# Kernel optimization log

Measured on AMD Instinct MI355X. Metric: run time of the kernel, lower is better.

Reference implementation:

```python
import jax, jax.numpy as jnp
import numpy as np

COMMITMENT_COST = 0.25


def l2norm(x, eps=1e-12):
    # F.normalize along last dim
    n = jnp.linalg.norm(x, axis=-1, keepdims=True)
    return x / jnp.maximum(n, eps)


def vector_quantize(x, codebook, commitment_cost):
    """Euclidean VQ: cdist + argmin, straight-through, VQ loss + perplexity.
    x: (B, N, D), codebook: (K, D)."""
    B, N, D = x.shape
    K = codebook.shape[0]
    flat = x.reshape(-1, D)  # (BN, D)
    # squared euclidean distances via expansion (no (BN,K,D) intermediate)
    d = (jnp.sum(flat * flat, axis=-1, keepdims=True)
         - 2.0 * flat @ codebook.T
         + jnp.sum(codebook * codebook, axis=-1))  # (BN, K)
    idx = jnp.argmin(d, axis=-1)  # (BN,)
    q = codebook[idx]  # (BN, D)
    # VQ losses
    e_latent = jnp.mean((jax.lax.stop_gradient(q) - flat) ** 2)
    q_latent = jnp.mean((q - jax.lax.stop_gradient(flat)) ** 2)
    loss = q_latent + commitment_cost * e_latent
    # perplexity over codebook usage (bincount, not dense one-hot)
    counts = jnp.zeros((K,), flat.dtype).at[idx].add(1.0)
    probs = counts / idx.shape[0]
    perplexity = jnp.exp(-jnp.sum(probs * jnp.log(probs + 1e-10)))
    return idx.reshape(B, N), perplexity, loss


def transform_mfcc(X):
    # wave_embedding.transform_freq: normalize frames, then rfft -> real -> bins 2:40
    Xn = l2norm(X)
    spec = jnp.fft.rfft(Xn, axis=-1).real[..., 2:40]  # (B, N, 38)
    return l2norm(spec)  # mfcc_embedding.norm_fn


def setup_inputs() -> dict:
    key = jax.random.key(0)
    k1, k2, k3 = jax.random.split(key, 3)
    X = jax.random.normal(k1, (16, 4096, 80), dtype=jnp.float32)
    wave_codebook = jax.random.normal(k2, (1024, 80), dtype=jnp.float32)
    mfcc_codebook = jax.random.normal(k3, (256, 38), dtype=jnp.float32)
    return {"X": X, "wave_codebook": wave_codebook, "mfcc_codebook": mfcc_codebook}


def reference(X, wave_codebook, mfcc_codebook):
    K_wave = wave_codebook.shape[0]
    wave_idx, wave_ppl, wave_loss = vector_quantize(X, wave_codebook, COMMITMENT_COST)
    X_mfcc = transform_mfcc(X)
    mfcc_idx, mfcc_ppl, mfcc_loss = vector_quantize(X_mfcc, mfcc_codebook, COMMITMENT_COST)
    mfcc_idx = mfcc_idx + K_wave
    # rearrange stack([wave, mfcc], dim=1): 'b c n -> b (n c)' -> interleave per frame
    B, N = wave_idx.shape
    encodings = jnp.stack([wave_idx, mfcc_idx], axis=-1).reshape(B, 2 * N)
    return encodings, wave_ppl, wave_loss, mfcc_ppl, mfcc_loss
```

## Files before the change

kernel.cpp:

```cpp
#include <hip/hip_runtime.h>
#include <hip/hip_bf16.h>
#include <math.h>


#define NROWS 65536
#define DW    80
#define KW    1024
#define DM    38
#define KM    256

typedef __attribute__((ext_vector_type(8))) short bf16x8;
typedef __attribute__((ext_vector_type(4))) float f32x4;

__device__ __forceinline__ void bf16split(float v, short& h, short& l) {
    __hip_bfloat16 hb = __float2bfloat16(v);
    float hf = __bfloat162float(hb);
    __hip_bfloat16 lb = __float2bfloat16(v - hf);
    h = *(short*)&hb;
    l = *(short*)&lb;
}

__device__ __forceinline__ void bf16split3(float v, short& a, short& b, short& c) {
    __hip_bfloat16 h = __float2bfloat16(v);
    float hf = __bfloat162float(h);
    float r = v - hf;
    __hip_bfloat16 m = __float2bfloat16(r);
    float mf = __bfloat162float(m);
    __hip_bfloat16 lo = __float2bfloat16(r - mf);
    a = *(short*)&h; b = *(short*)&m; c = *(short*)&lo;
}

__device__ __forceinline__ bf16x8 bf8zero() {
    bf16x8 z;
    #pragma unroll
    for (int j = 0; j < 8; ++j) z[j] = 0;
    return z;
}

__device__ __forceinline__ void wvq_tile(
    const bf16x8 (&Ah)[4][3], const bf16x8 (&Al)[4][3],
    const bf16x8 (&bh)[3], const bf16x8 (&bl)[3],
    float cnv, int idx0, float (&bd)[4][4], int (&bi)[4][4])
{
    f32x4 aL[4], aH[4];
    #pragma unroll
    for (int rt = 0; rt < 4; ++rt) {
        aL[rt] = (f32x4){0.f, 0.f, 0.f, 0.f};
        aH[rt] = (f32x4){0.f, 0.f, 0.f, 0.f};
    }
    #pragma unroll
    for (int s = 0; s < 3; ++s) {
        #pragma unroll
        for (int rt = 0; rt < 4; ++rt)
            aL[rt] = __builtin_amdgcn_mfma_f32_16x16x32_bf16(Al[rt][s], bl[s], aL[rt], 0, 0, 0);
        #pragma unroll
        for (int rt = 0; rt < 4; ++rt)
            aL[rt] = __builtin_amdgcn_mfma_f32_16x16x32_bf16(Ah[rt][s], bl[s], aL[rt], 0, 0, 0);
        #pragma unroll
        for (int rt = 0; rt < 4; ++rt)
            aH[rt] = __builtin_amdgcn_mfma_f32_16x16x32_bf16(Al[rt][s], bh[s], aH[rt], 0, 0, 0);
        #pragma unroll
        for (int rt = 0; rt < 4; ++rt)
            aH[rt] = __builtin_amdgcn_mfma_f32_16x16x32_bf16(Ah[rt][s], bh[s], aH[rt], 0, 0, 0);
    }
    #pragma unroll
    for (int rt = 0; rt < 4; ++rt)
        #pragma unroll
        for (int i = 0; i < 4; ++i) {
            float d = fmaf(-2.f, aL[rt][i] + aH[rt][i], cnv);
            if (d < bd[rt][i]) { bd[rt][i] = d; bi[rt][i] = idx0; }
        }
}

#define WS_SUMS   0
#define WS_HIST   256
#define WS_CNW    5376
#define WS_CNM    9472
#define WS_CTF    10496
#define WS_CBF    33536
#define WS_CWH    107264
#define WS_CWL    303872

__global__ __launch_bounds__(256) void prep_kernel(
    const float* __restrict__ cbw, const float* __restrict__ cbm,
    float* __restrict__ sums, int* __restrict__ hist,
    float* __restrict__ cn_w, float* __restrict__ cn_m,
    short* __restrict__ ctf, short* __restrict__ cbf,
    short* __restrict__ cwh, short* __restrict__ cwl)
{
    int idx = blockIdx.x * 256 + threadIdx.x;
    if (idx < 12288) {
        const int f = idx;
        const int ct = f / 192, rem = f % 192, s = rem >> 6, l = rem & 63;
        const int code = ct * 16 + (l & 15);
        const int k0 = 32 * s + 8 * (l >> 4);
        bf16x8 h, lo;
        if (k0 < DW) {
            const float4* p = (const float4*)(cbw + (size_t)code * DW + k0);
            float4 u = p[0], v = p[1];
            float fv[8] = {u.x, u.y, u.z, u.w, v.x, v.y, v.z, v.w};
            #pragma unroll
            for (int j = 0; j < 8; ++j) {
                short hh, ll;
                bf16split(fv[j], hh, ll);
                h[j] = hh; lo[j] = ll;
            }
        } else { h = bf8zero(); lo = bf8zero(); }
        *(bf16x8*)&cwh[(size_t)f * 8] = h;
        *(bf16x8*)&cwl[(size_t)f * 8] = lo;
    } else if (idx < 16128) {
        int t = idx - 12288;
        int col, k;
        if (t < 3072) {
            int j = t & 7, l = (t >> 3) & 63, tt = t >> 9;
            col = (tt >> 1) * 16 + (l & 15);
            k = 32 * (tt & 1) + 8 * (l >> 4) + j;
        } else {
            int i2 = t - 3072;
            int j = i2 & 7, l = (i2 >> 3) & 31, ct = i2 >> 8;
            col = ct * 16 + (l & 15);
            k = 64 + 8 * (l >> 4) + j;
        }
        float v = (col < DM)
            ? (float)cos(2.0 * 3.14159265358979323846 * (double)((col + 2) * k) / 80.0)
            : 0.f;
        short a, b, c; bf16split3(v, a, b, c);
        ctf[t] = a; ctf[3840 + t] = b; ctf[7680 + t] = c;
    } else if (idx < 28416) {
        int i3 = idx - 16128;
        int code, k;
        if (i3 < 8192) {
            int j = i3 & 7, l = (i3 >> 3) & 63, ct = i3 >> 9;
            code = ct * 16 + (l & 15);
            k = 8 * (l >> 4) + j;
        } else {
            int i4 = i3 - 8192;
            int j = i4 & 7, l = (i4 >> 3) & 31, ct = i4 >> 8;
            code = ct * 16 + (l & 15);
            k = 32 + 8 * (l >> 4) + j;
        }
        float v = (k < DM) ? cbm[(size_t)code * DM + k] : 0.f;
        short a, b, c; bf16split3(v, a, b, c);
        cbf[i3] = a; cbf[12288 + i3] = b; cbf[24576 + i3] = c;
    } else if (idx < 29440) {
        int i = idx - 28416;
        const float* p = cbw + (size_t)i * DW;
        float s = 0.f;
        for (int k = 0; k < DW; ++k) s = fmaf(p[k], p[k], s);
        cn_w[i] = s;
    } else if (idx < 29696) {
        int i = idx - 29440;
        const float* p = cbm + (size_t)i * DM;
        float s = 0.f;
        for (int j = 0; j < DM; ++j) s = fmaf(p[j], p[j], s);
        cn_m[i] = s;
    } else if (idx < 30976) {
        hist[idx - 29696] = 0;
    } else if (idx == 30976) sums[0] = 0.f;
    else if (idx == 30977)   sums[1] = 0.f;
}

__global__ __launch_bounds__(256, 2) void wave_vq_mfma(
    const float* __restrict__ X, const short* __restrict__ cwh,
    const short* __restrict__ cwl, const float* __restrict__ cn,
    float* __restrict__ out, float* __restrict__ sums)
{
    __shared__ float sd[2][64][16];
    __shared__ int   si[2][64][16];
    __shared__ float redw[2];

    const int tid  = threadIdx.x;
    const int l    = tid & 63;
    const int qu   = tid >> 6;
    const int grp  = qu >> 1;
    const int half = qu & 1;
    const int c16  = l & 15;
    const int g    = l >> 4;
    const size_t rowbase = (size_t)blockIdx.x * 128 + (size_t)grp * 64;

    bf16x8 Ah[4][3], Al[4][3];
    float xs2[4] = {0.f, 0.f, 0.f, 0.f};
    #pragma unroll
    for (int rt = 0; rt < 4; ++rt) {
        #pragma unroll
        for (int s = 0; s < 3; ++s) {
            const int k0 = 32 * s + 8 * g;
            bf16x8 ah, al;
            if (k0 < DW) {
                const float4* ap =
                    (const float4*)(X + (rowbase + rt * 16 + c16) * DW + k0);
                float4 u = ap[0], w = ap[1];
                float f[8] = {u.x, u.y, u.z, u.w, w.x, w.y, w.z, w.w};
                #pragma unroll
                for (int j = 0; j < 8; ++j) {
                    short hh, ll;
                    bf16split(f[j], hh, ll);
                    ah[j] = hh; al[j] = ll;
                    xs2[rt] = fmaf(f[j], f[j], xs2[rt]);
                }
            } else {
                ah = bf8zero(); al = bf8zero();
            }
            Ah[rt][s] = ah; Al[rt][s] = al;
        }
    }
    #pragma unroll
    for (int rt = 0; rt < 4; ++rt) {
        xs2[rt] += __shfl_xor(xs2[rt], 16, 64);
        xs2[rt] += __shfl_xor(xs2[rt], 32, 64);
    }

    float bd[4][4];
    int   bi[4][4];
    #pragma unroll
    for (int rt = 0; rt < 4; ++rt)
        #pragma unroll
        for (int i = 0; i < 4; ++i) { bd[rt][i] = 3.4e38f; bi[rt][i] = 0; }

    const bf16x8* Hp = (const bf16x8*)cwh + l;
    const bf16x8* Lp = (const bf16x8*)cwl + l;
    const int ct0 = half * 32;

    bf16x8 b0h[3], b0l[3], b1h[3], b1l[3];
    float cn0, cn1;
    #pragma unroll
    for (int s = 0; s < 3; ++s) {
        b0h[s] = Hp[(ct0 * 3 + s) * 64];
        b0l[s] = Lp[(ct0 * 3 + s) * 64];
    }
    cn0 = cn[ct0 * 16 + c16];

    #pragma unroll 1
    for (int ctl = 0; ctl < 32; ctl += 2) {
        const int ct = ct0 + ctl;
        #pragma unroll
        for (int s = 0; s < 3; ++s) {
            b1h[s] = Hp[((ct + 1) * 3 + s) * 64];
            b1l[s] = Lp[((ct + 1) * 3 + s) * 64];
        }
        cn1 = cn[(ct + 1) * 16 + c16];
        wvq_tile(Ah, Al, b0h, b0l, cn0, ct * 16 + c16, bd, bi);
        if (ctl + 2 < 32) {
            #pragma unroll
            for (int s = 0; s < 3; ++s) {
                b0h[s] = Hp[((ct + 2) * 3 + s) * 64];
                b0l[s] = Lp[((ct + 2) * 3 + s) * 64];
            }
            cn0 = cn[(ct + 2) * 16 + c16];
        }
        wvq_tile(Ah, Al, b1h, b1l, cn1, (ct + 1) * 16 + c16, bd, bi);
    }

    if (half == 1) {
        #pragma unroll
        for (int rt = 0; rt < 4; ++rt)
            #pragma unroll
            for (int i = 0; i < 4; ++i) {
                sd[grp][l][rt * 4 + i] = bd[rt][i];
                si[grp][l][rt * 4 + i] = bi[rt][i];
            }
    }
    __syncthreads();
    if (half == 0) {
        float lw = 0.f;
        #pragma unroll
        for (int rt = 0; rt < 4; ++rt) {
            #pragma unroll
            for (int i = 0; i < 4; ++i) {
                float d = bd[rt][i]; int ix = bi[rt][i];
                float dp = sd[grp][l][rt * 4 + i];
                int   ip = si[grp][l][rt * 4 + i];
                if (dp < d || (dp == d && ip < ix)) { d = dp; ix = ip; }
                #pragma unroll
                for (int m = 1; m < 16; m <<= 1) {
                    float d2 = __shfl_xor(d, m, 64);
                    int   i2 = __shfl_xor(ix, m, 64);
                    if (d2 < d || (d2 == d && i2 < ix)) { d = d2; ix = i2; }
                }
                float xn = __shfl(xs2[rt], (l & 48) + 4 * (l >> 4) + i, 64);
                if (c16 == 0) {
                    size_t row = rowbase + rt * 16 + 4 * g + i;
                    out[2 * row] = (float)ix;
                    lw += d + xn;
                }
            }
        }
        #pragma unroll
        for (int m = 1; m < 64; m <<= 1) lw += __shfl_xor(lw, m, 64);
        if (l == 0) redw[grp] = lw;
    }
    __syncthreads();
    if (tid == 0) atomicAdd(&sums[0], redw[0] + redw[1]);
}

__global__ __launch_bounds__(256, 2) void mfcc_mfma(
    const float* __restrict__ X, const float* __restrict__ cn_m,
    const short* __restrict__ ctf, const short* __restrict__ cbf,
    float* __restrict__ out, float* __restrict__ sums)
{
    __shared__ float XF[2][64 * 49];
    __shared__ float sd[2][64][16];
    __shared__ int   si[2][64][16];
    __shared__ float CN[KM];
    __shared__ float red2[2];

    const int tid  = threadIdx.x;
    const int l    = tid & 63;
    const int qu   = tid >> 6;
    const int grp  = qu >> 1;
    const int half = qu & 1;
    const int c16  = l & 15;
    const int g    = l >> 4;
    const size_t rowbase = (size_t)blockIdx.x * 128 + (size_t)grp * 64;

    CN[tid] = cn_m[tid];

    float* xfl = &XF[grp][0];

    #pragma unroll 1
    for (int rt2 = 0; rt2 < 2; ++rt2) {
        const int rt = half * 2 + rt2;
        bf16x8 A0[3], A1[3], A2[3];
        #pragma unroll
        for (int s = 0; s < 3; ++s) {
            const int k0 = 32 * s + 8 * g;
            if (k0 < DW) {
                const float4* ap =
                    (const float4*)(X + (rowbase + rt * 16 + c16) * DW + k0);
                float4 u = ap[0], v = ap[1];
                float f[8] = {u.x, u.y, u.z, u.w, v.x, v.y, v.z, v.w};
                bf16x8 a0, a1, a2;
                #pragma unroll
                for (int j = 0; j < 8; ++j) {
                    short aa, bb, cc;
                    bf16split3(f[j], aa, bb, cc);
                    a0[j] = aa; a1[j] = bb; a2[j] = cc;
                }
                A0[s] = a0; A1[s] = a1; A2[s] = a2;
            } else {
                A0[s] = bf8zero(); A1[s] = bf8zero(); A2[s] = bf8zero();
            }
        }

        f32x4 accA[3], accB[3];
        #pragma unroll
        for (int ct = 0; ct < 3; ++ct) {
            accA[ct] = (f32x4){0.f, 0.f, 0.f, 0.f};
            accB[ct] = (f32x4){0.f, 0.f, 0.f, 0.f};
        }

        #pragma unroll
        for (int s = 0; s < 3; ++s) {
            #pragma unroll
            for (int ct = 0; ct < 3; ++ct) {
                bf16x8 b0, b1, b2;
                if (s < 2) {
                    const int off = ((ct * 2 + s) * 64 + l) * 8;
                    b0 = *(const bf16x8*)&ctf[off];
                    b1 = *(const bf16x8*)&ctf[3840 + off];
                    b2 = *(const bf16x8*)&ctf[7680 + off];
                } else if (l < 32) {
                    const int off = 3072 + (ct * 32 + l) * 8;
                    b0 = *(const bf16x8*)&ctf[off];
                    b1 = *(const bf16x8*)&ctf[3840 + off];
                    b2 = *(const bf16x8*)&ctf[7680 + off];
                } else {
                    b0 = bf8zero(); b1 = bf8zero(); b2 = bf8zero();
                }
                accA[ct] = __builtin_amdgcn_mfma_f32_16x16x32_bf16(A2[s], b0, accA[ct], 0, 0, 0);
                accA[ct] = __builtin_amdgcn_mfma_f32_16x16x32_bf16(A1[s], b1, accA[ct], 0, 0, 0);
                accA[ct] = __builtin_amdgcn_mfma_f32_16x16x32_bf16(A0[s], b2, accA[ct], 0, 0, 0);
                accB[ct] = __builtin_amdgcn_mfma_f32_16x16x32_bf16(A1[s], b0, accB[ct], 0, 0, 0);
                accB[ct] = __builtin_amdgcn_mfma_f32_16x16x32_bf16(A0[s], b1, accB[ct], 0, 0, 0);
                accB[ct] = __builtin_amdgcn_mfma_f32_16x16x32_bf16(A0[s], b0, accB[ct], 0, 0, 0);
            }
        }

        f32x4 acc[3];
        #pragma unroll
        for (int ct = 0; ct < 3; ++ct) acc[ct] = accA[ct] + accB[ct];

        #pragma unroll
        for (int i = 0; i < 4; ++i) {
            float n2 = acc[0][i] * acc[0][i];
            n2 = fmaf(acc[1][i], acc[1][i], n2);
            n2 = fmaf(acc[2][i], acc[2][i], n2);
            #pragma unroll
            for (int m = 1; m < 16; m <<= 1) n2 += __shfl_xor(n2, m, 64);
            float inv = 1.0f / fmaxf(sqrtf(n2), 1e-12f);
            const int row_l = rt * 16 + 4 * g + i;
            #pragma unroll
            for (int ct = 0; ct < 3; ++ct)
                xfl[row_l * 49 + ct * 16 + c16] = acc[ct][i] * inv;
        }
    }
    __syncthreads();

    bf16x8 X0[4][3], X1[4][3];
    #pragma unroll
    for (int rt = 0; rt < 4; ++rt) {
        const int r0 = rt * 16 + c16;
        {
            const float* p = &xfl[r0 * 49 + 8 * g];
            bf16x8 q0, q1, q2;
            #pragma unroll
            for (int j = 0; j < 8; ++j) {
                short aa, bb, cc;
                bf16split3(p[j], aa, bb, cc);
                q0[j] = aa; q1[j] = bb; q2[j] = cc;
            }
            X0[rt][0] = q0; X0[rt][1] = q1; X0[rt][2] = q2;
        }
        if (g < 2) {
            const float* p = &xfl[r0 * 49 + 32 + 8 * g];
            bf16x8 q0, q1, q2;
            #pragma unroll
            for (int j = 0; j < 8; ++j) {
                short aa, bb, cc;
                bf16split3(p[j], aa, bb, cc);
                q0[j] = aa; q1[j] = bb; q2[j] = cc;
            }
            X1[rt][0] = q0; X1[rt][1] = q1; X1[rt][2] = q2;
        } else {
            X1[rt][0] = bf8zero(); X1[rt][1] = bf8zero(); X1[rt][2] = bf8zero();
        }
    }

    float bd[4][4];
    int   bi[4][4];
    #pragma unroll
    for (int rt = 0; rt < 4; ++rt)
        #pragma unroll
        for (int i = 0; i < 4; ++i) { bd[rt][i] = 3.4e38f; bi[rt][i] = 0; }

    #pragma unroll 1
    for (int ctl = 0; ctl < 8; ++ctl) {
        const int ct = half * 8 + ctl;
        bf16x8 B0[3], B1[3];
        const int off0 = (ct * 64 + l) * 8;
        B0[0] = *(const bf16x8*)&cbf[off0];
        B0[1] = *(const bf16x8*)&cbf[12288 + off0];
        B0[2] = *(const bf16x8*)&cbf[24576 + off0];
        if (l < 32) {
            const int off1 = 8192 + (ct * 32 + l) * 8;
            B1[0] = *(const bf16x8*)&cbf[off1];
            B1[1] = *(const bf16x8*)&cbf[12288 + off1];
            B1[2] = *(const bf16x8*)&cbf[24576 + off1];
        } else {
            B1[0] = bf8zero(); B1[1] = bf8zero(); B1[2] = bf8zero();
        }
        const float cnv = CN[ct * 16 + c16];
        const int idxbase = ct * 16 + c16;
        #pragma unroll
        for (int rt = 0; rt < 4; ++rt) {
            f32x4 p0 = (f32x4){0.f, 0.f, 0.f, 0.f};
            f32x4 q0 = (f32x4){0.f, 0.f, 0.f, 0.f};
            f32x4 p1 = (f32x4){0.f, 0.f, 0.f, 0.f};
            f32x4 q1 = (f32x4){0.f, 0.f, 0.f, 0.f};
            p0 = __builtin_amdgcn_mfma_f32_16x16x32_bf16(X0[rt][2], B0[0], p0, 0, 0, 0);
            p0 = __builtin_amdgcn_mfma_f32_16x16x32_bf16(X0[rt][1], B0[1], p0, 0, 0, 0);
            p0 = __builtin_amdgcn_mfma_f32_16x16x32_bf16(X0[rt][0], B0[2], p0, 0, 0, 0);
            q0 = __builtin_amdgcn_mfma_f32_16x16x32_bf16(X0[rt][1], B0[0], q0, 0, 0, 0);
            q0 = __builtin_amdgcn_mfma_f32_16x16x32_bf16(X0[rt][0], B0[1], q0, 0, 0, 0);
            q0 = __builtin_amdgcn_mfma_f32_16x16x32_bf16(X0[rt][0], B0[0], q0, 0, 0, 0);
            p1 = __builtin_amdgcn_mfma_f32_16x16x32_bf16(X1[rt][2], B1[0], p1, 0, 0, 0);
            p1 = __builtin_amdgcn_mfma_f32_16x16x32_bf16(X1[rt][1], B1[1], p1, 0, 0, 0);
            p1 = __builtin_amdgcn_mfma_f32_16x16x32_bf16(X1[rt][0], B1[2], p1, 0, 0, 0);
            q1 = __builtin_amdgcn_mfma_f32_16x16x32_bf16(X1[rt][1], B1[0], q1, 0, 0, 0);
            q1 = __builtin_amdgcn_mfma_f32_16x16x32_bf16(X1[rt][0], B1[1], q1, 0, 0, 0);
            q1 = __builtin_amdgcn_mfma_f32_16x16x32_bf16(X1[rt][0], B1[0], q1, 0, 0, 0);
            #pragma unroll
            for (int i = 0; i < 4; ++i) {
                float d = fmaf(-2.f, (p0[i] + q0[i]) + (p1[i] + q1[i]), cnv);
                if (d < bd[rt][i]) { bd[rt][i] = d; bi[rt][i] = idxbase; }
            }
        }
    }

    if (half == 1) {
        #pragma unroll
        for (int rt = 0; rt < 4; ++rt)
            #pragma unroll
            for (int i = 0; i < 4; ++i) {
                sd[grp][l][rt * 4 + i] = bd[rt][i];
                si[grp][l][rt * 4 + i] = bi[rt][i];
            }
    }
    __syncthreads();
    if (half == 0) {
        float lm = 0.f;
        #pragma unroll
        for (int rt = 0; rt < 4; ++rt) {
            #pragma unroll
            for (int i = 0; i < 4; ++i) {
                float d = bd[rt][i]; int ix = bi[rt][i];
                float dp = sd[grp][l][rt * 4 + i];
                int   ip = si[grp][l][rt * 4 + i];
                if (dp < d || (dp == d && ip < ix)) { d = dp; ix = ip; }
                #pragma unroll
                for (int m = 1; m < 16; m <<= 1) {
                    float d2 = __shfl_xor(d, m, 64);
                    int   i2 = __shfl_xor(ix, m, 64);
                    if (d2 < d || (d2 == d && i2 < ix)) { d = d2; ix = i2; }
                }
                if (c16 == 0) {
                    size_t row = rowbase + rt * 16 + 4 * g + i;
                    out[2 * row + 1] = (float)(ix + KW);
                    lm += d + 1.0f;
                }
            }
        }
        #pragma unroll
        for (int m = 1; m < 64; m <<= 1) lm += __shfl_xor(lm, m, 64);
        if (l == 0) red2[grp] = lm;
    }
    __syncthreads();
    if (tid == 0) atomicAdd(&sums[1], red2[0] + red2[1]);
}

__global__ __launch_bounds__(256) void hist_kernel(
    const float* __restrict__ out, int* __restrict__ hist)
{
    __shared__ int h[1280];
    const int tid = threadIdx.x;
    for (int i = tid; i < 1280; i += 256) h[i] = 0;
    __syncthreads();
    const int r = blockIdx.x * 256 + tid;
    float2 e = *(const float2*)&out[2 * r];
    atomicAdd(&h[(int)e.x], 1);
    atomicAdd(&h[1024 + ((int)e.y - KW)], 1);
    __syncthreads();
    for (int i = tid; i < 1280; i += 256)
        if (h[i]) atomicAdd(&hist[i], h[i]);
}

__global__ __launch_bounds__(256) void finalize_kernel(
    const int* __restrict__ hist, const float* __restrict__ sums,
    float* __restrict__ out)
{
    __shared__ float red[4];
    const int tid = threadIdx.x;
    const bool wv = (blockIdx.x == 0);
    const int K = wv ? KW : KM;
    const int base = wv ? 0 : 1024;
    float s = 0.f;
    for (int i = tid; i < K; i += 256) {
        float p = (float)hist[base + i] * (1.0f / 65536.0f);
        s += p * logf(p + 1e-10f);
    }
    #pragma unroll
    for (int off = 32; off >= 1; off >>= 1) s += __shfl_xor(s, off, 64);
    if ((tid & 63) == 0) red[tid >> 6] = s;
    __syncthreads();
    if (tid == 0) {
        float t = red[0] + red[1] + red[2] + red[3];
        float ppl = expf(-t);
        float denom = wv ? (float)(NROWS * DW) : (float)(NROWS * DM);
        int obase = 2 * NROWS + (wv ? 0 : 2);
        out[obase]     = ppl;
        out[obase + 1] = 1.25f * sums[wv ? 0 : 1] / denom;
    }
}

extern "C" void kernel_launch(void* const* d_in, const int* in_sizes, int n_in,
                              void* d_out, int out_size, void* d_ws, size_t ws_size,
                              hipStream_t stream) {
    const float* X   = (const float*)d_in[0];
    const float* cbw = (const float*)d_in[1];
    const float* cbm = (const float*)d_in[2];
    float* out = (float*)d_out;

    char* ws = (char*)d_ws;
    float* sums = (float*)(ws + WS_SUMS);
    int*   hist = (int*)(ws + WS_HIST);
    float* cn_w = (float*)(ws + WS_CNW);
    float* cn_m = (float*)(ws + WS_CNM);
    short* ctf  = (short*)(ws + WS_CTF);
    short* cbf  = (short*)(ws + WS_CBF);
    short* cwh  = (short*)(ws + WS_CWH);
    short* cwl  = (short*)(ws + WS_CWL);

    prep_kernel<<<122, 256, 0, stream>>>(cbw, cbm, sums, hist, cn_w, cn_m,
                                         ctf, cbf, cwh, cwl);
    wave_vq_mfma<<<NROWS / 128, 256, 0, stream>>>(X, cwh, cwl, cn_w, out, sums);
    mfcc_mfma<<<NROWS / 128, 256, 0, stream>>>(X, cn_m, ctf, cbf, out, sums);
    hist_kernel<<<NROWS / 256, 256, 0, stream>>>(out, hist);
    finalize_kernel<<<2, 256, 0, stream>>>(hist, sums, out);
}
```

Measured before the change: 95.28 us.

## Stage wave codebook tiles in LDS and split rows across all four waves

The wave VQ kernel no longer splits the codebook between two half-waves per 64-row group. Each of the four waves now owns 32 rows and scans the full codebook. Codebook hi/lo tiles are loaded cooperatively into shared memory in chunks of four column tiles, with register prefetch of the next chunk. This removes redundant per-wave global codebook loads and the cross-half LDS argmin merge. In exchange it adds per-chunk block barriers and halves the rows per wave, which lowers MFMA reuse of each loaded B fragment.

```diff
diff --git a/kernel.cpp b/kernel.cpp
--- a/kernel.cpp
+++ b/kernel.cpp
@@ -37,34 +37,34 @@
     return z;
 }
 
-__device__ __forceinline__ void wvq_tile(
-    const bf16x8 (&Ah)[4][3], const bf16x8 (&Al)[4][3],
+__device__ __forceinline__ void wvq_tile2(
+    const bf16x8 (&Ah)[2][3], const bf16x8 (&Al)[2][3],
     const bf16x8 (&bh)[3], const bf16x8 (&bl)[3],
-    float cnv, int idx0, float (&bd)[4][4], int (&bi)[4][4])
+    float cnv, int idx0, float (&bd)[2][4], int (&bi)[2][4])
 {
-    f32x4 aL[4], aH[4];
-    #pragma unroll
-    for (int rt = 0; rt < 4; ++rt) {
+    f32x4 aL[2], aH[2];
+    #pragma unroll
+    for (int rt = 0; rt < 2; ++rt) {
         aL[rt] = (f32x4){0.f, 0.f, 0.f, 0.f};
         aH[rt] = (f32x4){0.f, 0.f, 0.f, 0.f};
     }
     #pragma unroll
     for (int s = 0; s < 3; ++s) {
         #pragma unroll
-        for (int rt = 0; rt < 4; ++rt)
+        for (int rt = 0; rt < 2; ++rt)
             aL[rt] = __builtin_amdgcn_mfma_f32_16x16x32_bf16(Al[rt][s], bl[s], aL[rt], 0, 0, 0);
         #pragma unroll
-        for (int rt = 0; rt < 4; ++rt)
+        for (int rt = 0; rt < 2; ++rt)
             aL[rt] = __builtin_amdgcn_mfma_f32_16x16x32_bf16(Ah[rt][s], bl[s], aL[rt], 0, 0, 0);
         #pragma unroll
-        for (int rt = 0; rt < 4; ++rt)
+        for (int rt = 0; rt < 2; ++rt)
             aH[rt] = __builtin_amdgcn_mfma_f32_16x16x32_bf16(Al[rt][s], bh[s], aH[rt], 0, 0, 0);
         #pragma unroll
-        for (int rt = 0; rt < 4; ++rt)
+        for (int rt = 0; rt < 2; ++rt)
             aH[rt] = __builtin_amdgcn_mfma_f32_16x16x32_bf16(Ah[rt][s], bh[s], aH[rt], 0, 0, 0);
     }
     #pragma unroll
-    for (int rt = 0; rt < 4; ++rt)
+    for (int rt = 0; rt < 2; ++rt)
         #pragma unroll
         for (int i = 0; i < 4; ++i) {
             float d = fmaf(-2.f, aL[rt][i] + aH[rt][i], cnv);
@@ -165,23 +165,21 @@
     const short* __restrict__ cwl, const float* __restrict__ cn,
     float* __restrict__ out, float* __restrict__ sums)
 {
-    __shared__ float sd[2][64][16];
-    __shared__ int   si[2][64][16];
-    __shared__ float redw[2];
-
-    const int tid  = threadIdx.x;
-    const int l    = tid & 63;
-    const int qu   = tid >> 6;
-    const int grp  = qu >> 1;
-    const int half = qu & 1;
-    const int c16  = l & 15;
-    const int g    = l >> 4;
-    const size_t rowbase = (size_t)blockIdx.x * 128 + (size_t)grp * 64;
-
-    bf16x8 Ah[4][3], Al[4][3];
-    float xs2[4] = {0.f, 0.f, 0.f, 0.f};
-    #pragma unroll
-    for (int rt = 0; rt < 4; ++rt) {
+    __shared__ int4 LH4[768];
+    __shared__ int4 LL4[768];
+    __shared__ float redw[4];
+
+    const int tid = threadIdx.x;
+    const int l   = tid & 63;
+    const int qu  = tid >> 6;
+    const int c16 = l & 15;
+    const int g   = l >> 4;
+    const size_t rowbase = (size_t)blockIdx.x * 128 + (size_t)qu * 32;
+
+    bf16x8 Ah[2][3], Al[2][3];
+    float xs2[2] = {0.f, 0.f};
+    #pragma unroll
+    for (int rt = 0; rt < 2; ++rt) {
         #pragma unroll
         for (int s = 0; s < 3; ++s) {
             const int k0 = 32 * s + 8 * g;
@@ -205,92 +203,92 @@
         }
     }
     #pragma unroll
-    for (int rt = 0; rt < 4; ++rt) {
+    for (int rt = 0; rt < 2; ++rt) {
         xs2[rt] += __shfl_xor(xs2[rt], 16, 64);
         xs2[rt] += __shfl_xor(xs2[rt], 32, 64);
     }
 
-    float bd[4][4];
-    int   bi[4][4];
-    #pragma unroll
-    for (int rt = 0; rt < 4; ++rt)
+    float bd[2][4];
+    int   bi[2][4];
+    #pragma unroll
+    for (int rt = 0; rt < 2; ++rt)
         #pragma unroll
         for (int i = 0; i < 4; ++i) { bd[rt][i] = 3.4e38f; bi[rt][i] = 0; }
 
-    const bf16x8* Hp = (const bf16x8*)cwh + l;
-    const bf16x8* Lp = (const bf16x8*)cwl + l;
-    const int ct0 = half * 32;
-
-    bf16x8 b0h[3], b0l[3], b1h[3], b1l[3];
-    float cn0, cn1;
-    #pragma unroll
-    for (int s = 0; s < 3; ++s) {
-        b0h[s] = Hp[(ct0 * 3 + s) * 64];
-        b0l[s] = Lp[(ct0 * 3 + s) * 64];
-    }
-    cn0 = cn[ct0 * 16 + c16];
+    const int4* Hg = (const int4*)cwh;
+    const int4* Lg = (const int4*)cwl;
+
+    int4 rh[3], rl[3];
+    #pragma unroll
+    for (int i = 0; i < 3; ++i) {
+        rh[i] = Hg[i * 256 + tid];
+        rl[i] = Lg[i * 256 + tid];
+    }
+    #pragma unroll
+    for (int i = 0; i < 3; ++i) {
+        LH4[i * 256 + tid] = rh[i];
+        LL4[i * 256 + tid] = rl[i];
+    }
+    __syncthreads();
 
     #pragma unroll 1
-    for (int ctl = 0; ctl < 32; ctl += 2) {
-        const int ct = ct0 + ctl;
-        #pragma unroll
-        for (int s = 0; s < 3; ++s) {
-            b1h[s] = Hp[((ct + 1) * 3 + s) * 64];
-            b1l[s] = Lp[((ct + 1) * 3 + s) * 64];
-        }
-        cn1 = cn[(ct + 1) * 16 + c16];
-        wvq_tile(Ah, Al, b0h, b0l, cn0, ct * 16 + c16, bd, bi);
-        if (ctl + 2 < 32) {
+    for (int c = 0; c < 16; ++c) {
+        if (c + 1 < 16) {
+            #pragma unroll
+            for (int i = 0; i < 3; ++i) {
+                rh[i] = Hg[(c + 1) * 768 + i * 256 + tid];
+                rl[i] = Lg[(c + 1) * 768 + i * 256 + tid];
+            }
+        }
+        #pragma unroll
+        for (int t = 0; t < 4; ++t) {
+            const int ct = c * 4 + t;
+            bf16x8 bh[3], bl[3];
             #pragma unroll
             for (int s = 0; s < 3; ++s) {
-                b0h[s] = Hp[((ct + 2) * 3 + s) * 64];
-                b0l[s] = Lp[((ct + 2) * 3 + s) * 64];
-            }
-            cn0 = cn[(ct + 2) * 16 + c16];
-        }
-        wvq_tile(Ah, Al, b1h, b1l, cn1, (ct + 1) * 16 + c16, bd, bi);
-    }
-
-    if (half == 1) {
-        #pragma unroll
-        for (int rt = 0; rt < 4; ++rt)
-            #pragma unroll
-            for (int i = 0; i < 4; ++i) {
-                sd[grp][l][rt * 4 + i] = bd[rt][i];
-                si[grp][l][rt * 4 + i] = bi[rt][i];
-            }
-    }
-    __syncthreads();
-    if (half == 0) {
-        float lw = 0.f;
-        #pragma unroll
-        for (int rt = 0; rt < 4; ++rt) {
-            #pragma unroll
-            for (int i = 0; i < 4; ++i) {
-                float d = bd[rt][i]; int ix = bi[rt][i];
-                float dp = sd[grp][l][rt * 4 + i];
-                int   ip = si[grp][l][rt * 4 + i];
-                if (dp < d || (dp == d && ip < ix)) { d = dp; ix = ip; }
-                #pragma unroll
-                for (int m = 1; m < 16; m <<= 1) {
-                    float d2 = __shfl_xor(d, m, 64);
-                    int   i2 = __shfl_xor(ix, m, 64);
-                    if (d2 < d || (d2 == d && i2 < ix)) { d = d2; ix = i2; }
-                }
-                float xn = __shfl(xs2[rt], (l & 48) + 4 * (l >> 4) + i, 64);
-                if (c16 == 0) {
-                    size_t row = rowbase + rt * 16 + 4 * g + i;
-                    out[2 * row] = (float)ix;
-                    lw += d + xn;
-                }
-            }
-        }
-        #pragma unroll
-        for (int m = 1; m < 64; m <<= 1) lw += __shfl_xor(lw, m, 64);
-        if (l == 0) redw[grp] = lw;
-    }
-    __syncthreads();
-    if (tid == 0) atomicAdd(&sums[0], redw[0] + redw[1]);
+                bh[s] = *(const bf16x8*)&LH4[(t * 3 + s) * 64 + l];
+                bl[s] = *(const bf16x8*)&LL4[(t * 3 + s) * 64 + l];
+            }
+            const float cnv = cn[ct * 16 + c16];
+            wvq_tile2(Ah, Al, bh, bl, cnv, ct * 16 + c16, bd, bi);
+        }
+        __syncthreads();
+        if (c + 1 < 16) {
+            #pragma unroll
+            for (int i = 0; i < 3; ++i) {
+                LH4[i * 256 + tid] = rh[i];
+                LL4[i * 256 + tid] = rl[i];
+            }
+            __syncthreads();
+        }
+    }
+
+    float lw = 0.f;
+    #pragma unroll
+    for (int rt = 0; rt < 2; ++rt) {
+        #pragma unroll
+        for (int i = 0; i < 4; ++i) {
+            float d = bd[rt][i]; int ix = bi[rt][i];
+            #pragma unroll
+            for (int m = 1; m < 16; m <<= 1) {
+                float d2 = __shfl_xor(d, m, 64);
+                int   i2 = __shfl_xor(ix, m, 64);
+                if (d2 < d || (d2 == d && i2 < ix)) { d = d2; ix = i2; }
+            }
+            float xn = __shfl(xs2[rt], (l & 48) + 4 * g + i, 64);
+            if (c16 == 0) {
+                size_t row = rowbase + rt * 16 + 4 * g + i;
+                out[2 * row] = (float)ix;
+                lw += d + xn;
+            }
+        }
+    }
+    #pragma unroll
+    for (int m = 1; m < 64; m <<= 1) lw += __shfl_xor(lw, m, 64);
+    if (l == 0) redw[qu] = lw;
+    __syncthreads();
+    if (tid == 0)
+        atomicAdd(&sums[0], redw[0] + redw[1] + redw[2] + redw[3]);
 }
 
 __global__ __launch_bounds__(256, 2) void mfcc_mfma(
```

Result: slower. 117.6 us (+23.4%).
